# Performance work log

Measured on AMD Instinct MI355X. Metric: run time of the kernel, lower is better.

Reference implementation:

```python
import jax, jax.numpy as jnp
import numpy as np

N_EMBD = 1024
N_HEAD = 16
HEAD_DIM = N_EMBD // N_HEAD
BLOCK = 2048
BATCH = 2


def setup_inputs() -> dict:
    key = jax.random.key(0)
    ks = jax.random.split(key, 6)
    s_in = 1.0 / np.sqrt(N_EMBD)
    s_hd = 1.0 / np.sqrt(N_EMBD)  # fan-in of c_proj1 is n_head*head_dim = n_embd
    return {
        "x": jax.random.normal(ks[0], (BATCH, BLOCK, N_EMBD), jnp.float32),
        "wq": jax.random.normal(ks[1], (N_EMBD, N_HEAD, HEAD_DIM), jnp.float32) * s_in,
        "wk": jax.random.normal(ks[2], (N_EMBD, N_HEAD, HEAD_DIM), jnp.float32) * s_in,
        "wv": jax.random.normal(ks[3], (N_EMBD, N_HEAD, HEAD_DIM), jnp.float32) * s_in,
        "wp1": jax.random.normal(ks[4], (N_HEAD, HEAD_DIM, N_EMBD), jnp.float32) * s_hd,
        "wp2": jax.random.normal(ks[5], (N_EMBD, N_EMBD), jnp.float32) * s_in,
    }


def reference(x, wq, wk, wv, wp1, wp2):
    # QKV projections: DenseGeneral(features=(H, D), axis=-1), no bias
    q = jnp.einsum('btc,chd->bthd', x, wq)
    k = jnp.einsum('btc,chd->bthd', x, wk)
    v = jnp.einsum('btc,chd->bthd', x, wv)
    scale = HEAD_DIM ** (-0.5)
    wei = jnp.einsum('bqhd,bkhd->bhqk', q, k) * scale  # [B,H,T,T]
    tril = jnp.tril(jnp.ones((BLOCK, BLOCK), dtype=bool))
    wei = jnp.where(tril, wei, -jnp.inf)
    wei = jax.nn.softmax(wei, axis=-1)
    att = jnp.einsum('bhqk,bkhd->bqhd', wei, v)  # [B,T,H,D]
    # c_proj1: DenseGeneral over (-2,-1) -> contract (H,D)
    y = jnp.einsum('bqhd,hdc->bqc', att, wp1)
    # c_proj2: Dense
    out = jnp.einsum('bqc,ce->bqe', y, wp2)
    return out
```

## Files before the change

### kernel.cpp

```cpp
#include <hip/hip_runtime.h>
#include <hip/hip_bf16.h>
#include <stdint.h>

typedef __bf16 bf16;
typedef __bf16 bf16x4 __attribute__((ext_vector_type(4)));
typedef __bf16 bf16x8 __attribute__((ext_vector_type(8)));
typedef float  f32x4  __attribute__((ext_vector_type(4)));

#define MFMA16(a,b,c) __builtin_amdgcn_mfma_f32_16x16x32_bf16((a),(b),(c),0,0,0)

#define TSEQ 2048
#define NE   1024
#define NE3  3072
#define NH   16
#define HD   64
#define MTOK 4096

#define EXP2F(x) exp2f(x)

__device__ __forceinline__ void gl_lds16(const bf16* g, bf16* l) {
  __builtin_amdgcn_global_load_lds(
      (const __attribute__((address_space(1))) void*)g,
      (__attribute__((address_space(3))) void*)l,
      16, 0, 0);
}

__global__ void k_cast(const float* __restrict__ in, bf16* __restrict__ out, int n4) {
  int i = blockIdx.x * blockDim.x + threadIdx.x;
  if (i < n4) {
    float4 v = reinterpret_cast<const float4*>(in)[i];
    bf16x4 o = { (bf16)v.x, (bf16)v.y, (bf16)v.z, (bf16)v.w };
    reinterpret_cast<bf16x4*>(out)[i] = o;
  }
}

__global__ void k_transpose_all(const float* __restrict__ wq, const float* __restrict__ wk,
                                const float* __restrict__ wv, const float* __restrict__ wp2,
                                bf16* __restrict__ W3T, bf16* __restrict__ Wp2T) {
  __shared__ float tile[64][65];
  const int z = blockIdx.z;
  const float* in = (z == 0) ? wq : (z == 1) ? wk : (z == 2) ? wv : wp2;
  bf16* out = (z < 3) ? (W3T + (size_t)z * 1024 * 1024) : Wp2T;
  const int r0 = blockIdx.y * 64, c0 = blockIdx.x * 64;
  const int lc = threadIdx.x & 63, lr0 = threadIdx.x >> 6;
#pragma unroll
  for (int i = 0; i < 16; ++i) {
    int lr = i*4 + lr0;
    tile[lr][lc] = in[(size_t)(r0 + lr) * 1024 + (c0 + lc)];
  }
  __syncthreads();
#pragma unroll
  for (int i = 0; i < 16; ++i) {
    int lr = i*4 + lr0;
    out[(size_t)(c0 + lr) * 1024 + (r0 + lc)] = (bf16)tile[lc][lr];
  }
}

__global__ void k_transpose_v(const bf16* __restrict__ V, bf16* __restrict__ Vt) {
  __shared__ bf16 tile[64][65];
  const int b = blockIdx.z, h = blockIdx.y, t0 = blockIdx.x * 64;
  const int lc = threadIdx.x & 63, lr0 = threadIdx.x >> 6;
#pragma unroll
  for (int i = 0; i < 16; ++i) {
    int lr = i*4 + lr0;
    tile[lr][lc] = V[(size_t)(b*TSEQ + t0 + lr)*NE3 + h*HD + lc];
  }
  __syncthreads();
#pragma unroll
  for (int i = 0; i < 16; ++i) {
    int lr = i*4 + lr0;
    Vt[((size_t)(b*NH + h)*HD + lr)*TSEQ + t0 + lc] = tile[lc][lr];
  }
}

template<int BN, typename OutT>
__global__ __launch_bounds__(256) void k_gemm_bt(const bf16* __restrict__ A,
                                                 const bf16* __restrict__ Bt,
                                                 OutT* __restrict__ C,
                                                 const int M, const int N, const int K) {
  constexpr int NC = BN / 32;
  __shared__ bf16 As[2][128*32];
  __shared__ bf16 Bs[2][BN*32];
  const int tid  = threadIdx.x;
  const int lane = tid & 63;
  const int wave = tid >> 6;
  const int wr = (wave >> 1) * 64;
  const int wc = (wave & 1) * (BN/2);
  const int l15 = lane & 15;
  const int l4  = lane >> 4;

  const int nwg = gridDim.x * gridDim.y;
  int id = blockIdx.y * gridDim.x + blockIdx.x;
  id = (id & 7) * (nwg >> 3) + (id >> 3);
  const int bm = (id / gridDim.x) * 128;
  const int bn = (id % gridDim.x) * BN;

  const int srow = tid >> 2;
  const int scol = ((tid & 3) ^ ((tid >> 3) & 3)) * 8;
  const bf16* ag = A  + (size_t)(bm + srow) * K + scol;
  const bf16* bg = Bt + (size_t)(bn + srow) * K + scol;
  const int kx = (l4 ^ ((l15 >> 1) & 3)) * 8;

  f32x4 acc[4][NC] = {};

  auto stage = [&](int buf, int k0) {
    bf16* al = As[buf] + tid * 8;
    bf16* bl = Bs[buf] + tid * 8;
    gl_lds16(ag + k0,                   al);
    gl_lds16(ag + k0 + (size_t)64 * K,  al + 64*32);
    gl_lds16(bg + k0,                   bl);
    if (BN == 128) gl_lds16(bg + k0 + (size_t)64 * K, bl + 64*32);
  };

  stage(0, 0);
  __syncthreads();
  int cur = 0;
  for (int k0 = 0; k0 < K; k0 += 32) {
    if (k0 + 32 < K) stage(cur ^ 1, k0 + 32);
    bf16x8 af[4], bfr[NC];
#pragma unroll
    for (int m = 0; m < 4; ++m)
      af[m] = *reinterpret_cast<const bf16x8*>(&As[cur][(wr + m*16 + l15)*32 + kx]);
#pragma unroll
    for (int n = 0; n < NC; ++n)
      bfr[n] = *reinterpret_cast<const bf16x8*>(&Bs[cur][(wc + n*16 + l15)*32 + kx]);
#pragma unroll
    for (int m = 0; m < 4; ++m)
#pragma unroll
      for (int n = 0; n < NC; ++n)
        acc[m][n] = MFMA16(af[m], bfr[n], acc[m][n]);
    __syncthreads();
    cur ^= 1;
  }

#pragma unroll
  for (int m = 0; m < 4; ++m) {
    const int row = bm + wr + m*16 + l4*4;
#pragma unroll
    for (int n = 0; n < NC; ++n) {
      const int col = bn + wc + n*16 + l15;
#pragma unroll
      for (int r = 0; r < 4; ++r)
        C[(size_t)(row + r) * N + col] = (OutT)acc[m][n][r];
    }
  }
}

__global__ __launch_bounds__(256) void k_attn(const bf16* __restrict__ QKV,
                                              const bf16* __restrict__ Vt,
                                              bf16* __restrict__ O) {
  __shared__ bf16 Ks[2][2*64*32];
  __shared__ bf16 Vs[2][2*64*32];
  __shared__ bf16 Ps[4][2*16*32];

  const int tid  = threadIdx.x;
  const int lane = tid & 63;
  const int wave = tid >> 6;
  const int l15 = lane & 15;
  const int l4  = lane >> 4;

  const int x  = blockIdx.x;
  const int p  = x >> 5;
  const int bh = x & 31;
  const int b  = bh >> 4, h = bh & 15;

  const bf16* Qb = QKV + (size_t)b*TSEQ*NE3 +        h*HD;
  const bf16* Kb = QKV + (size_t)b*TSEQ*NE3 + 1024 + h*HD;
  const bf16* Vb = Vt  + (size_t)bh*HD*TSEQ;
  bf16* Pw = Ps[wave];

  const float SC = 0.125f * 1.44269504f;
  const int swz = (l4 ^ ((l15 >> 1) & 3)) * 8;
  const int sr = tid >> 2;
  const int sg = tid & 3;
  const int g  = sg ^ ((sr >> 1) & 3);

  auto stage = [&](int buf, int t) {
#pragma unroll
    for (int ks = 0; ks < 2; ++ks)
      gl_lds16(&Kb[(size_t)(t*64 + sr)*NE3 + ks*32 + g*8], &Ks[buf][ks*2048 + tid*8]);
#pragma unroll
    for (int ks = 0; ks < 2; ++ks)
      gl_lds16(&Vb[(size_t)sr*TSEQ + t*64 + ks*32 + g*8],  &Vs[buf][ks*2048 + tid*8]);
  };

  stage(0, 0);
  __syncthreads();
  int cur = 0;
  int i = 0;

  for (int ci = 0; ci < 2; ++ci) {
    const int c  = ci ? (31 - p) : p;
    const int qw = c*64 + wave*16;

    bf16x8 qf[2];
#pragma unroll
    for (int ks = 0; ks < 2; ++ks) {
      bf16x8 qv = *reinterpret_cast<const bf16x8*>(
          &Qb[(size_t)(qw + l15)*NE3 + ks*32 + l4*8]);
#pragma unroll
      for (int j = 0; j < 8; ++j) qv[j] = (bf16)((float)qv[j] * SC);
      qf[ks] = qv;
    }

    f32x4 ot[4] = {};
    float m_run = -1e30f;
    float l_part = 0.f;

    const int ntc = c + 1;
    for (int t = 0; t < ntc; ++t, ++i) {
      if (i + 1 < 33) {
        const int nt2 = (i + 1 <= p) ? (i + 1) : (i - p);
        stage(cur ^ 1, nt2);
      }

      f32x4 st[4] = {};
#pragma unroll
      for (int kvf = 0; kvf < 4; ++kvf) {
        const int row = kvf*16 + l15;
#pragma unroll
        for (int ks = 0; ks < 2; ++ks) {
          bf16x8 kf = *reinterpret_cast<const bf16x8*>(&Ks[cur][ks*2048 + row*32 + swz]);
          st[kvf] = MFMA16(kf, qf[ks], st[kvf]);
        }
      }

      const int q = qw + l15;
      if (t == c) {
#pragma unroll
        for (int kvf = 0; kvf < 4; ++kvf)
#pragma unroll
          for (int r = 0; r < 4; ++r)
            if (t*64 + kvf*16 + l4*4 + r > q) st[kvf][r] = -1e30f;
      }

      float mx = st[0][0];
#pragma unroll
      for (int kvf = 0; kvf < 4; ++kvf)
#pragma unroll
        for (int r = 0; r < 4; ++r) mx = fmaxf(mx, st[kvf][r]);
      mx = fmaxf(mx, __shfl_xor(mx, 16));
      mx = fmaxf(mx, __shfl_xor(mx, 32));

      if (__any(mx > m_run + 8.f)) {
        const float mnew = fmaxf(m_run, mx);
        const float corr = EXP2F(m_run - mnew);
        l_part *= corr;
#pragma unroll
        for (int n2 = 0; n2 < 4; ++n2) ot[n2] *= corr;
        m_run = mnew;
      }

      float rs = 0.f;
#pragma unroll
      for (int kvf = 0; kvf < 4; ++kvf) {
        bf16x4 pk;
#pragma unroll
        for (int r = 0; r < 4; ++r) {
          const float pv = EXP2F(st[kvf][r] - m_run);
          rs += pv;
          pk[r] = (bf16)pv;
        }
        const int gp = (((kvf & 1)*2 + (l4 >> 1)) ^ ((l15 >> 1) & 3));
        *reinterpret_cast<bf16x4*>(
            &Pw[(kvf>>1)*512 + l15*32 + gp*8 + (l4 & 1)*4]) = pk;
      }
      l_part += rs;

      bf16x8 pa[2];
#pragma unroll
      for (int ks = 0; ks < 2; ++ks)
        pa[ks] = *reinterpret_cast<const bf16x8*>(&Pw[ks*512 + l15*32 + swz]);
#pragma unroll
      for (int n2 = 0; n2 < 4; ++n2) {
        const int vrow = n2*16 + l15;
#pragma unroll
        for (int ks = 0; ks < 2; ++ks) {
          bf16x8 vf = *reinterpret_cast<const bf16x8*>(&Vs[cur][ks*2048 + vrow*32 + swz]);
          ot[n2] = MFMA16(vf, pa[ks], ot[n2]);
        }
      }

      __syncthreads();
      cur ^= 1;
    }

    float l = l_part;
    l += __shfl_xor(l, 16);
    l += __shfl_xor(l, 32);
    const float rl = 1.f / l;
    const size_t row = (size_t)(b*TSEQ + qw + l15);
#pragma unroll
    for (int n2 = 0; n2 < 4; ++n2) {
      bf16x4 ov;
#pragma unroll
      for (int r = 0; r < 4; ++r) ov[r] = (bf16)(ot[n2][r] * rl);
      *reinterpret_cast<bf16x4*>(&O[row*NE + h*HD + n2*16 + l4*4]) = ov;
    }
  }
}

extern "C" void kernel_launch(void* const* d_in, const int* in_sizes, int n_in,
                              void* d_out, int out_size, void* d_ws, size_t ws_size,
                              hipStream_t stream) {
  const float* x   = (const float*)d_in[0];
  const float* wq  = (const float*)d_in[1];
  const float* wk  = (const float*)d_in[2];
  const float* wv  = (const float*)d_in[3];
  const float* wp1 = (const float*)d_in[4];
  const float* wp2 = (const float*)d_in[5];
  float* out = (float*)d_out;

  char* ws = (char*)d_ws;
  const size_t MB = 1024ull * 1024ull;
  bf16* xb   = (bf16*)(ws + 0*MB);
  bf16* W3T  = (bf16*)(ws + 8*MB);
  bf16* wp1b = (bf16*)(ws + 14*MB);
  bf16* wp2T = (bf16*)(ws + 16*MB);
  bf16* WcT  = (bf16*)(ws + 18*MB);
  bf16* QKVb = (bf16*)(ws + 20*MB);
  bf16* Vtb  = (bf16*)(ws + 44*MB);
  bf16* attb = (bf16*)(ws + 52*MB);

  k_cast<<<4096, 256, 0, stream>>>(x, xb, MTOK*NE/4);
  k_cast<<<1024, 256, 0, stream>>>(wp1, wp1b, 1024*1024/4);
  k_transpose_all<<<dim3(16, 16, 4), 256, 0, stream>>>(wq, wk, wv, wp2, W3T, wp2T);

  k_gemm_bt<128, bf16><<<dim3(8, 8), 256, 0, stream>>>(wp2T, wp1b, WcT, 1024, 1024, 1024);

  k_gemm_bt<128, bf16><<<dim3(24, 32), 256, 0, stream>>>(xb, W3T, QKVb, MTOK, NE3, NE);

  k_transpose_v<<<dim3(TSEQ/64, NH, 2), 256, 0, stream>>>(QKVb + 2048, Vtb);

  k_attn<<<dim3(512), 256, 0, stream>>>(QKVb, Vtb, attb);

  k_gemm_bt<128, float><<<dim3(8, 32), 256, 0, stream>>>(attb, WcT, out, MTOK, NE, NE);
}
```

Baseline: 148.7 us.

## Enlarge attention tiles to 128, use hardware exp2, fuse wp1 cast into transpose

The attention kernel moves from 64-row to 128-row query/key tiles, running 512 threads (8 waves) per block on 256 blocks. This doubles K/V reuse per staged tile and halves the number of tile iterations and barriers. Softmax exp2 now calls the raw hardware exp instruction, skipping the libm range handling. The wp1 cast is folded into the weight-transpose launch, and the weight-product GEMM uses a 64-wide tile to spread over more blocks. The trade-off is larger LDS use and more registers per thread, with fewer resident blocks.

```diff
diff --git a/kernel.cpp b/kernel.cpp
--- a/kernel.cpp
+++ b/kernel.cpp
@@ -16,7 +16,14 @@
 #define HD   64
 #define MTOK 4096
 
-#define EXP2F(x) exp2f(x)
+#if defined(__has_builtin) && __has_builtin(__builtin_amdgcn_exp2f)
+#define EXP2F(x) __builtin_amdgcn_exp2f(x)
+#else
+__device__ __forceinline__ float exp2_fast(float x) {
+  float r; asm("v_exp_f32 %0, %1" : "=v"(r) : "v"(x)); return r;
+}
+#define EXP2F(x) exp2_fast(x)
+#endif
 
 __device__ __forceinline__ void gl_lds16(const bf16* g, bf16* l) {
   __builtin_amdgcn_global_load_lds(
@@ -36,13 +43,23 @@
 
 __global__ void k_transpose_all(const float* __restrict__ wq, const float* __restrict__ wk,
                                 const float* __restrict__ wv, const float* __restrict__ wp2,
-                                bf16* __restrict__ W3T, bf16* __restrict__ Wp2T) {
+                                const float* __restrict__ wp1,
+                                bf16* __restrict__ W3T, bf16* __restrict__ Wp2T,
+                                bf16* __restrict__ Wp1b) {
   __shared__ float tile[64][65];
   const int z = blockIdx.z;
+  const int r0 = blockIdx.y * 64, c0 = blockIdx.x * 64;
+  const int lc = threadIdx.x & 63, lr0 = threadIdx.x >> 6;
+  if (z == 4) {
+#pragma unroll
+    for (int i = 0; i < 16; ++i) {
+      int lr = i*4 + lr0;
+      Wp1b[(size_t)(r0 + lr)*1024 + c0 + lc] = (bf16)wp1[(size_t)(r0 + lr)*1024 + c0 + lc];
+    }
+    return;
+  }
   const float* in = (z == 0) ? wq : (z == 1) ? wk : (z == 2) ? wv : wp2;
   bf16* out = (z < 3) ? (W3T + (size_t)z * 1024 * 1024) : Wp2T;
-  const int r0 = blockIdx.y * 64, c0 = blockIdx.x * 64;
-  const int lc = threadIdx.x & 63, lr0 = threadIdx.x >> 6;
 #pragma unroll
   for (int i = 0; i < 16; ++i) {
     int lr = i*4 + lr0;
@@ -146,12 +163,12 @@
   }
 }
 
-__global__ __launch_bounds__(256) void k_attn(const bf16* __restrict__ QKV,
+__global__ __launch_bounds__(512) void k_attn(const bf16* __restrict__ QKV,
                                               const bf16* __restrict__ Vt,
                                               bf16* __restrict__ O) {
-  __shared__ bf16 Ks[2][2*64*32];
-  __shared__ bf16 Vs[2][2*64*32];
-  __shared__ bf16 Ps[4][2*16*32];
+  __shared__ bf16 Ks[2][2*128*32];
+  __shared__ bf16 Vs[2][4*64*32];
+  __shared__ bf16 Ps[8][4*16*32];
 
   const int tid  = threadIdx.x;
   const int lane = tid & 63;
@@ -171,17 +188,25 @@
 
   const float SC = 0.125f * 1.44269504f;
   const int swz = (l4 ^ ((l15 >> 1) & 3)) * 8;
-  const int sr = tid >> 2;
-  const int sg = tid & 3;
-  const int g  = sg ^ ((sr >> 1) & 3);
+  const int key = (l15 >> 1) & 3;
+
+  const int krow = tid >> 2;
+  const int kg   = (tid & 3) ^ ((krow >> 1) & 3);
+  const int vd   = (tid >> 2) & 63;
+  const int vg   = (tid & 3) ^ ((vd >> 1) & 3);
+  const int vp0  = tid >> 8;
 
   auto stage = [&](int buf, int t) {
 #pragma unroll
-    for (int ks = 0; ks < 2; ++ks)
-      gl_lds16(&Kb[(size_t)(t*64 + sr)*NE3 + ks*32 + g*8], &Ks[buf][ks*2048 + tid*8]);
-#pragma unroll
-    for (int ks = 0; ks < 2; ++ks)
-      gl_lds16(&Vb[(size_t)sr*TSEQ + t*64 + ks*32 + g*8],  &Vs[buf][ks*2048 + tid*8]);
+    for (int kk = 0; kk < 2; ++kk)
+      gl_lds16(&Kb[(size_t)(t*128 + krow)*NE3 + kk*32 + kg*8],
+               &Ks[buf][kk*4096 + tid*8]);
+#pragma unroll
+    for (int kk = 0; kk < 2; ++kk) {
+      const int ksv = kk*2 + vp0;
+      gl_lds16(&Vb[(size_t)vd*TSEQ + t*128 + ksv*32 + vg*8],
+               &Vs[buf][kk*4096 + tid*8]);
+    }
   };
 
   stage(0, 0);
@@ -190,8 +215,8 @@
   int i = 0;
 
   for (int ci = 0; ci < 2; ++ci) {
-    const int c  = ci ? (31 - p) : p;
-    const int qw = c*64 + wave*16;
+    const int c  = ci ? (15 - p) : p;
+    const int qw = c*128 + wave*16;
 
     bf16x8 qf[2];
 #pragma unroll
@@ -207,36 +232,35 @@
     float m_run = -1e30f;
     float l_part = 0.f;
 
-    const int ntc = c + 1;
-    for (int t = 0; t < ntc; ++t, ++i) {
-      if (i + 1 < 33) {
-        const int nt2 = (i + 1 <= p) ? (i + 1) : (i - p);
-        stage(cur ^ 1, nt2);
-      }
-
-      f32x4 st[4] = {};
-#pragma unroll
-      for (int kvf = 0; kvf < 4; ++kvf) {
+    for (int t = 0; t <= c; ++t, ++i) {
+      if (i + 1 < 17) {
+        const int nxt = (i + 1 <= p) ? (i + 1) : (i - p);
+        stage(cur ^ 1, nxt);
+      }
+
+      f32x4 st[8];
+#pragma unroll
+      for (int kvf = 0; kvf < 8; ++kvf) {
+        st[kvf] = f32x4{0.f, 0.f, 0.f, 0.f};
         const int row = kvf*16 + l15;
 #pragma unroll
         for (int ks = 0; ks < 2; ++ks) {
-          bf16x8 kf = *reinterpret_cast<const bf16x8*>(&Ks[cur][ks*2048 + row*32 + swz]);
+          bf16x8 kf = *reinterpret_cast<const bf16x8*>(&Ks[cur][ks*4096 + row*32 + swz]);
           st[kvf] = MFMA16(kf, qf[ks], st[kvf]);
         }
       }
 
-      const int q = qw + l15;
       if (t == c) {
 #pragma unroll
-        for (int kvf = 0; kvf < 4; ++kvf)
+        for (int kvf = 0; kvf < 8; ++kvf)
 #pragma unroll
           for (int r = 0; r < 4; ++r)
-            if (t*64 + kvf*16 + l4*4 + r > q) st[kvf][r] = -1e30f;
+            if (kvf*16 + l4*4 + r > wave*16 + l15) st[kvf][r] = -1e30f;
       }
 
       float mx = st[0][0];
 #pragma unroll
-      for (int kvf = 0; kvf < 4; ++kvf)
+      for (int kvf = 0; kvf < 8; ++kvf)
 #pragma unroll
         for (int r = 0; r < 4; ++r) mx = fmaxf(mx, st[kvf][r]);
       mx = fmaxf(mx, __shfl_xor(mx, 16));
@@ -253,7 +277,7 @@
 
       float rs = 0.f;
 #pragma unroll
-      for (int kvf = 0; kvf < 4; ++kvf) {
+      for (int kvf = 0; kvf < 8; ++kvf) {
         bf16x4 pk;
 #pragma unroll
         for (int r = 0; r < 4; ++r) {
@@ -261,23 +285,23 @@
           rs += pv;
           pk[r] = (bf16)pv;
         }
-        const int gp = (((kvf & 1)*2 + (l4 >> 1)) ^ ((l15 >> 1) & 3));
+        const int gp = (((kvf & 1)*2 + (l4 >> 1)) ^ key);
         *reinterpret_cast<bf16x4*>(
             &Pw[(kvf>>1)*512 + l15*32 + gp*8 + (l4 & 1)*4]) = pk;
       }
       l_part += rs;
 
-      bf16x8 pa[2];
-#pragma unroll
-      for (int ks = 0; ks < 2; ++ks)
-        pa[ks] = *reinterpret_cast<const bf16x8*>(&Pw[ks*512 + l15*32 + swz]);
+      bf16x8 pa[4];
+#pragma unroll
+      for (int ksv = 0; ksv < 4; ++ksv)
+        pa[ksv] = *reinterpret_cast<const bf16x8*>(&Pw[ksv*512 + l15*32 + swz]);
 #pragma unroll
       for (int n2 = 0; n2 < 4; ++n2) {
         const int vrow = n2*16 + l15;
 #pragma unroll
-        for (int ks = 0; ks < 2; ++ks) {
-          bf16x8 vf = *reinterpret_cast<const bf16x8*>(&Vs[cur][ks*2048 + vrow*32 + swz]);
-          ot[n2] = MFMA16(vf, pa[ks], ot[n2]);
+        for (int ksv = 0; ksv < 4; ++ksv) {
+          bf16x8 vf = *reinterpret_cast<const bf16x8*>(&Vs[cur][ksv*2048 + vrow*32 + swz]);
+          ot[n2] = MFMA16(vf, pa[ksv], ot[n2]);
         }
       }
 
@@ -323,16 +347,16 @@
   bf16* attb = (bf16*)(ws + 52*MB);
 
   k_cast<<<4096, 256, 0, stream>>>(x, xb, MTOK*NE/4);
-  k_cast<<<1024, 256, 0, stream>>>(wp1, wp1b, 1024*1024/4);
-  k_transpose_all<<<dim3(16, 16, 4), 256, 0, stream>>>(wq, wk, wv, wp2, W3T, wp2T);
-
-  k_gemm_bt<128, bf16><<<dim3(8, 8), 256, 0, stream>>>(wp2T, wp1b, WcT, 1024, 1024, 1024);
+  k_transpose_all<<<dim3(16, 16, 5), 256, 0, stream>>>(wq, wk, wv, wp2, wp1,
+                                                       W3T, wp2T, wp1b);
+
+  k_gemm_bt<64, bf16><<<dim3(16, 8), 256, 0, stream>>>(wp2T, wp1b, WcT, 1024, 1024, 1024);
 
   k_gemm_bt<128, bf16><<<dim3(24, 32), 256, 0, stream>>>(xb, W3T, QKVb, MTOK, NE3, NE);
 
   k_transpose_v<<<dim3(TSEQ/64, NH, 2), 256, 0, stream>>>(QKVb + 2048, Vtb);
 
-  k_attn<<<dim3(512), 256, 0, stream>>>(QKVb, Vtb, attb);
+  k_attn<<<dim3(256), 512, 0, stream>>>(QKVb, Vtb, attb);
 
   k_gemm_bt<128, float><<<dim3(8, 32), 256, 0, stream>>>(attb, WcT, out, MTOK, NE, NE);
 }
```

Measured after the change: 128.4 us. -13.7%, faster.
